# Kernel optimization log

Hardware: AMD Instinct MI355X
Metric: run time of the kernel (lower is better)

Reference implementation:

```python
import jax, jax.numpy as jnp
import numpy as np

PENALTY_B = 1.0


def setup_inputs() -> dict:
    key = jax.random.key(0)
    B = jax.random.uniform(key, (8192, 16384), dtype=jnp.float32)
    return {"B": B}


def reference(B):
    # loss = PenaltyB * mean_i( max(0, sum_j B[i,j] - 1) )
    row_sums = jnp.sum(B, axis=1)                 # [batch]
    hinge = jnp.maximum(row_sums - 1.0, 0.0)      # [batch]
    return PENALTY_B * jnp.mean(hinge)
```

## Files before the change

### kernel.cpp

```cpp
#include <hip/hip_runtime.h>
#include <hip/hip_bf16.h>

#define ROWS 8192
#define COLS 16384
#define BLOCK 256

__global__ __launch_bounds__(BLOCK) void row_hinge_kernel(const float* __restrict__ B,
                                                          float* __restrict__ ws) {
    const int row = blockIdx.x;
    const float4* rowp = (const float4*)(B + (size_t)row * COLS);
    const int tid = threadIdx.x;

    float s = 0.0f;
#pragma unroll
    for (int it = 0; it < (COLS / 4) / BLOCK; ++it) {
        float4 v = rowp[tid + it * BLOCK];
        s += (v.x + v.y) + (v.z + v.w);
    }

#pragma unroll
    for (int off = 32; off > 0; off >>= 1)
        s += __shfl_down(s, off, 64);

    __shared__ float wsum[BLOCK / 64];
    const int wave = tid >> 6;
    const int lane = tid & 63;
    if (lane == 0) wsum[wave] = s;
    __syncthreads();

    if (tid == 0) {
        float rs = 0.0f;
#pragma unroll
        for (int w = 0; w < BLOCK / 64; ++w) rs += wsum[w];
        float h = rs - 1.0f;
        ws[row] = h > 0.0f ? h : 0.0f;
    }
}

__global__ __launch_bounds__(BLOCK) void final_reduce_kernel(const float* __restrict__ ws,
                                                             float* __restrict__ out) {
    const int tid = threadIdx.x;
    float s = 0.0f;
#pragma unroll
    for (int i = tid; i < ROWS; i += BLOCK)
        s += ws[i];

#pragma unroll
    for (int off = 32; off > 0; off >>= 1)
        s += __shfl_down(s, off, 64);

    __shared__ float wsum[BLOCK / 64];
    const int wave = tid >> 6;
    const int lane = tid & 63;
    if (lane == 0) wsum[wave] = s;
    __syncthreads();

    if (tid == 0) {
        float total = 0.0f;
#pragma unroll
        for (int w = 0; w < BLOCK / 64; ++w) total += wsum[w];
        out[0] = total * (1.0f / (float)ROWS);
    }
}

extern "C" void kernel_launch(void* const* d_in, const int* in_sizes, int n_in,
                              void* d_out, int out_size, void* d_ws, size_t ws_size,
                              hipStream_t stream) {
    const float* B = (const float*)d_in[0];
    float* out = (float*)d_out;
    float* ws = (float*)d_ws;

    row_hinge_kernel<<<ROWS, BLOCK, 0, stream>>>(B, ws);
    final_reduce_kernel<<<1, BLOCK, 0, stream>>>(ws, out);
}
```

Before: 674.9 us.

## Assign one wavefront per row and vectorize final reduction loads

Each 64-lane wavefront now reduces a whole row, with four rows per block, so the grid shrinks by four. This removes the shared-memory cross-wave reduction and the __syncthreads. The final reduce kernel now reads the per-row workspace with float4 loads. Each wave issues a longer serial chain of loads (partially unrolled by 8), so each wave may expose more memory latency while the block-level sync goes away.

```diff
diff --git a/kernel.cpp b/kernel.cpp
--- a/kernel.cpp
+++ b/kernel.cpp
@@ -1,20 +1,22 @@
 #include <hip/hip_runtime.h>
-#include <hip/hip_bf16.h>
 
 #define ROWS 8192
 #define COLS 16384
 #define BLOCK 256
+#define WPB (BLOCK / 64)
+#define GRID (ROWS / WPB)
 
 __global__ __launch_bounds__(BLOCK) void row_hinge_kernel(const float* __restrict__ B,
                                                           float* __restrict__ ws) {
-    const int row = blockIdx.x;
+    const int wave = threadIdx.x >> 6;
+    const int lane = threadIdx.x & 63;
+    const int row  = blockIdx.x * WPB + wave;
     const float4* rowp = (const float4*)(B + (size_t)row * COLS);
-    const int tid = threadIdx.x;
 
     float s = 0.0f;
-#pragma unroll
-    for (int it = 0; it < (COLS / 4) / BLOCK; ++it) {
-        float4 v = rowp[tid + it * BLOCK];
+#pragma unroll 8
+    for (int it = 0; it < (COLS / 4) / 64; ++it) {
+        float4 v = rowp[lane + it * 64];
         s += (v.x + v.y) + (v.z + v.w);
     }
 
@@ -22,17 +24,8 @@
     for (int off = 32; off > 0; off >>= 1)
         s += __shfl_down(s, off, 64);
 
-    __shared__ float wsum[BLOCK / 64];
-    const int wave = tid >> 6;
-    const int lane = tid & 63;
-    if (lane == 0) wsum[wave] = s;
-    __syncthreads();
-
-    if (tid == 0) {
-        float rs = 0.0f;
-#pragma unroll
-        for (int w = 0; w < BLOCK / 64; ++w) rs += wsum[w];
-        float h = rs - 1.0f;
+    if (lane == 0) {
+        float h = s - 1.0f;
         ws[row] = h > 0.0f ? h : 0.0f;
     }
 }
@@ -40,10 +33,13 @@
 __global__ __launch_bounds__(BLOCK) void final_reduce_kernel(const float* __restrict__ ws,
                                                              float* __restrict__ out) {
     const int tid = threadIdx.x;
+    const float4* p = (const float4*)ws;
     float s = 0.0f;
 #pragma unroll
-    for (int i = tid; i < ROWS; i += BLOCK)
-        s += ws[i];
+    for (int it = 0; it < (ROWS / 4) / BLOCK; ++it) {
+        float4 v = p[tid + it * BLOCK];
+        s += (v.x + v.y) + (v.z + v.w);
+    }
 
 #pragma unroll
     for (int off = 32; off > 0; off >>= 1)
@@ -70,6 +66,6 @@
     float* out = (float*)d_out;
     float* ws = (float*)d_ws;
 
-    row_hinge_kernel<<<ROWS, BLOCK, 0, stream>>>(B, ws);
+    row_hinge_kernel<<<GRID, BLOCK, 0, stream>>>(B, ws);
     final_reduce_kernel<<<1, BLOCK, 0, stream>>>(ws, out);
 }
```

Result: no change. 670.1 us (-0.7%).
